# Kernel optimization log

Measured on AMD Instinct MI355X. Metric: run time of the kernel, lower is better.

## Reference

```python
import jax, jax.numpy as jnp
import numpy as np
from jax import lax

B, C_IN, C_MID, C_OUT, H, W = 8, 256, 128, 256, 128, 128
DN = ('NCHW', 'OIHW', 'NCHW')


def conv_bn(x, w, scale, shift, pad, relu):
    # conv (bias=False) + eval-mode BatchNorm folded to per-channel scale/shift
    y = lax.conv_general_dilated(x, w, (1, 1), [(pad, pad), (pad, pad)],
                                 dimension_numbers=DN)
    y = y * scale[None, :, None, None] + shift[None, :, None, None]
    return jax.nn.relu(y) if relu else y


def setup_inputs() -> dict:
    key = jax.random.key(0)
    ks = jax.random.split(key, 20)
    d = {"x": jax.random.normal(ks[0], (B, C_IN, H, W), dtype=jnp.float32)}
    f = 0.05  # weight scale
    def wparams(i, cout, cin, k):
        kk = jax.random.split(ks[i], 3)
        return (jax.random.normal(kk[0], (cout, cin, k, k), jnp.float32) * f,
                1.0 + 0.1 * jax.random.normal(kk[1], (cout,), jnp.float32),
                0.1 * jax.random.normal(kk[2], (cout,), jnp.float32))
    d["w_l"], d["s_l"], d["o_l"] = wparams(1, C_MID, C_IN, 3)
    d["w_r"], d["s_r"], d["o_r"] = wparams(2, C_MID, C_IN, 3)
    d["w_t"], d["s_t"], d["o_t"] = wparams(3, C_MID, C_IN, 3)
    d["w_b"], d["s_b"], d["o_b"] = wparams(4, C_MID, C_IN, 3)
    d["w2"], d["s2"], d["o2"] = wparams(5, C_OUT, C_MID, 3)
    d["w1"], d["s1"], d["o1"] = wparams(6, C_IN, C_IN, 1)
    return d


def reference(x, w_l, s_l, o_l, w_r, s_r, o_r, w_t, s_t, o_t,
              w_b, s_b, o_b, w2, s2, o2, w1, s1, o1):
    # four directional branches: conv+bn+relu then corner pooling (cummax scan)
    xl = lax.cummax(conv_bn(x, w_l, s_l, o_l, 1, True), axis=3, reverse=True)  # left: max over w'>=w
    xr = lax.cummax(conv_bn(x, w_r, s_r, o_r, 1, True), axis=3)                # right: max over w'<=w
    xt = lax.cummax(conv_bn(x, w_t, s_t, o_t, 1, True), axis=2, reverse=True)  # top: max over h'>=h
    xb = lax.cummax(conv_bn(x, w_b, s_b, o_b, 1, True), axis=2)                # bottom: max over h'<=h
    x1 = conv_bn(xl + xr + xb + xt, w2, s2, o2, 1, False)  # 3x3 conv+bn, no relu
    x2 = conv_bn(x, w1, s1, o1, 0, False)                  # 1x1 conv+bn skip, no relu
    return jax.nn.relu(x1 + x2)
```

## Files before the change

### kernel.cpp

```cpp
#include <hip/hip_runtime.h>

#define NEG_INF (-3.402823466e+38f)

typedef __bf16 bf16x8 __attribute__((ext_vector_type(8)));
typedef float  f32x16 __attribute__((ext_vector_type(16)));

__device__ __forceinline__ unsigned short f2bf(float f){
    unsigned u = __builtin_bit_cast(unsigned, f);
    u += 0x7fffu + ((u >> 16) & 1u);
    return (unsigned short)(u >> 16);
}
__device__ __forceinline__ float bf2f(unsigned short h){
    unsigned u = ((unsigned)h) << 16;
    return __builtin_bit_cast(float, u);
}

#if defined(__has_builtin)
#if __has_builtin(__builtin_amdgcn_global_load_lds)
#define ASYNC_CP 1
#endif
#endif

__device__ __forceinline__ void gl_lds(const unsigned short* g, unsigned short* lbase, int lane) {
#ifdef ASYNC_CP
    __builtin_amdgcn_global_load_lds(
        (const __attribute__((address_space(1))) unsigned int*)g,
        (__attribute__((address_space(3))) unsigned int*)lbase, 16, 0, 0);
#else
    *(uint4*)(lbase + (size_t)lane * 8) = *(const uint4*)g;
#endif
}

__global__ void __launch_bounds__(256)
k_xpose(const float* __restrict__ x, unsigned short* __restrict__ xh)
{
    __shared__ float tile[64 * 129];
    const int t = threadIdx.x;
    const int ci0 = blockIdx.x * 64, h = blockIdx.y, b = blockIdx.z;
    const float4* src = (const float4*)x;
#pragma unroll
    for (int i = 0; i < 8; ++i) {
        int idx = t + i * 256;
        int ci = idx >> 5, w4 = idx & 31;
        float4 v = src[((b * 256 + ci0 + ci) * 128 + h) * 32 + w4];
        tile[ci * 129 + w4 * 4 + 0] = v.x;
        tile[ci * 129 + w4 * 4 + 1] = v.y;
        tile[ci * 129 + w4 * 4 + 2] = v.z;
        tile[ci * 129 + w4 * 4 + 3] = v.w;
    }
    __syncthreads();
    unsigned* dst = (unsigned*)xh;
#pragma unroll
    for (int i = 0; i < 16; ++i) {
        int idx = t + i * 256;
        int w = idx >> 5, cp = idx & 31;
        float lo = tile[(cp * 2 + 0) * 129 + w];
        float hi = tile[(cp * 2 + 1) * 129 + w];
        dst[((b * 128 + h) * 128 + w) * 128 + (ci0 >> 1) + cp] =
            (unsigned)f2bf(lo) | ((unsigned)f2bf(hi) << 16);
    }
}

__global__ void __launch_bounds__(256)
k_wpack(const float* __restrict__ wl, const float* __restrict__ sl, const float* __restrict__ ol,
        const float* __restrict__ wr, const float* __restrict__ sr, const float* __restrict__ orr,
        const float* __restrict__ wt, const float* __restrict__ st, const float* __restrict__ ot,
        const float* __restrict__ wb, const float* __restrict__ sb, const float* __restrict__ ob,
        const float* __restrict__ w2, const float* __restrict__ s2, const float* __restrict__ o2,
        const float* __restrict__ w1, const float* __restrict__ s1, const float* __restrict__ o1,
        unsigned short* __restrict__ wpkBR, unsigned short* __restrict__ wpk2,
        unsigned short* __restrict__ wpk1, float* __restrict__ shF, float* __restrict__ obF)
{
    int i = blockIdx.x * 256 + threadIdx.x;
    if (i < 1179648) {
        int br = i / 294912, r = i % 294912;
        int c = r / 2304, r2 = r % 2304, ci = r2 / 9, k9 = r2 % 9;
        const float* wp = br == 0 ? wl : br == 1 ? wr : br == 2 ? wt : wb;
        const float* sp = br == 0 ? sl : br == 1 ? sr : br == 2 ? st : sb;
        float v = wp[r] * sp[c];
        int p = (c >> 4) * 64 + br * 16 + (c & 15);
        wpkBR[(((((ci >> 4) * 9 + k9) * 2 + ((ci >> 3) & 1)) * 512 + p) * 8) + (ci & 7)] = f2bf(v);
    } else if (i < 1474560) {
        int j = i - 1179648;
        int c = j / 1152, r2 = j % 1152, ci = r2 / 9, k9 = r2 % 9;
        wpk2[(((((ci >> 4) * 9 + k9) * 2 + ((ci >> 3) & 1)) * 256 + c) * 8) + (ci & 7)] = f2bf(w2[j] * s2[c]);
    } else if (i < 1540096) {
        int j = i - 1474560;
        int c = j >> 8, ci = j & 255;
        wpk1[((((ci >> 4) * 2 + ((ci >> 3) & 1)) * 256 + c) * 8) + (ci & 7)] = f2bf(w1[j] * s1[c]);
    } else if (i < 1540608) {
        int p = i - 1540096;
        int br = (p >> 4) & 3, c = (p >> 6) * 16 + (p & 15);
        const float* op = br == 0 ? ol : br == 1 ? orr : br == 2 ? ot : ob;
        shF[p] = op[c];
    } else if (i < 1540864) {
        int c = i - 1540608;
        obF[c] = o2[c] + o1[c];
    }
}

#define XIN_SH 12672
__global__ void __launch_bounds__(256, 2)
k_brconv(const unsigned short* __restrict__ xh, const unsigned short* __restrict__ wpkBR,
         const float* __restrict__ shF, unsigned short* __restrict__ sbuf2,
         unsigned short* __restrict__ ytbT, unsigned short* __restrict__ ytbB)
{
    __shared__ __align__(16) unsigned short smem[2 * XIN_SH + 128];
    unsigned short* xinA = smem;
    unsigned short* xinB = smem + XIN_SH;
    float* shs = (float*)(smem + 2 * XIN_SH);

    const int t = threadIdx.x;
    const int lin = (int)blockIdx.x + ((int)blockIdx.y << 3) + ((int)blockIdx.z << 8);
    const int swz = (lin & 7) * 256 + (lin >> 3);
    const int bx = swz & 7, h0 = ((swz >> 3) & 31) << 2, b = swz >> 8;
    const int wv = t >> 6, lane = t & 63;
    const int lo5 = lane & 31, hi1 = lane >> 5;
    const int hi32 = lane & 32;

    if (t < 64) shs[t] = shF[bx * 64 + t];
    for (int idx = t; idx < 3168; idx += 256)
        *(uint4*)(smem + idx * 8) = make_uint4(0, 0, 0, 0);

    f32x16 acc[2][4];
#pragma unroll
    for (int ct = 0; ct < 2; ++ct)
#pragma unroll
        for (int nb = 0; nb < 4; ++nb)
#pragma unroll
            for (int i = 0; i < 16; ++i) acc[ct][nb][i] = 0.f;

    __syncthreads();

    for (int s = wv; s < 24; s += 4) {
        int r = s >> 2, khi = (s >> 1) & 1, half = s & 1;
        int ih = h0 - 1 + r;
        if (ih >= 0 && ih < 128)
            gl_lds(xh + (((size_t)(b * 128 + ih) * 128 + half * 64 + lane) * 256) + khi * 8,
                   xinA + ((r * 2 + khi) * 132 + 1 + half * 64) * 8, lane);
    }
    __syncthreads();

    unsigned short* xcur = xinA;
    unsigned short* xnxt = xinB;

    for (int cb = 0; cb < 16; ++cb) {
        bf16x8 af0[9], af1[9];
        {
            const unsigned short* wp = wpkBR + ((size_t)(cb * 18 + hi1) * 512 + bx * 64) * 8;
#pragma unroll
            for (int k9 = 0; k9 < 9; ++k9) {
                af0[k9] = *(const bf16x8*)(wp + lo5 * 8);
                af1[k9] = *(const bf16x8*)(wp + (32 + lo5) * 8);
                wp += 8192;
            }
        }
        if (cb < 15) {
            const int nc = cb + 1;
            for (int s = wv; s < 24; s += 4) {
                int r = s >> 2, khi = (s >> 1) & 1, half = s & 1;
                int ih = h0 - 1 + r;
                if (ih >= 0 && ih < 128)
                    gl_lds(xh + (((size_t)(b * 128 + ih) * 128 + half * 64 + lane) * 256) + nc * 16 + khi * 8,
                           xnxt + ((r * 2 + khi) * 132 + 1 + half * 64) * 8, lane);
            }
        }
#pragma unroll
        for (int k9 = 0; k9 < 9; ++k9) {
            const int kh = k9 / 3, kw = k9 % 3;
#pragma unroll
            for (int nb = 0; nb < 4; ++nb) {
                bf16x8 bf = *(const bf16x8*)(xcur + (((wv + kh) * 2 + hi1) * 132 + nb * 32 + lo5 + kw) * 8);
                acc[0][nb] = __builtin_amdgcn_mfma_f32_32x32x16_bf16(af0[k9], bf, acc[0][nb], 0, 0, 0);
                acc[1][nb] = __builtin_amdgcn_mfma_f32_32x32x16_bf16(af1[k9], bf, acc[1][nb], 0, 0, 0);
            }
        }
        __syncthreads();
        unsigned short* tp = xcur; xcur = xnxt; xnxt = tp;
    }

    unsigned short* pbw = smem + wv * 3072;
    const int hg = h0 + wv;

#pragma unroll
    for (int r = 0; r < 8; ++r) {
        const int m = (r & 3) + 8 * (r >> 2) + 4 * hi1;
        const float shv = shs[m];
        float carry = NEG_INF;
#pragma unroll
        for (int nn = 3; nn >= 0; --nn) {
            float a = fmaxf(acc[0][nn][r] + shv, 0.f);
#pragma unroll
            for (int d = 1; d < 32; d <<= 1) {
                float o = __shfl_down(a, d);
                if (lo5 < 32 - d) a = fmaxf(a, o);
            }
            a = fmaxf(a, carry);
            carry = __shfl(a, hi32);
            acc[0][nn][r] = a;
        }
    }
#pragma unroll
    for (int r = 8; r < 16; ++r) {
        const int m = 16 + (r & 3) + 8 * ((r >> 2) & 1) + 4 * hi1;
        const float shv = shs[m];
        float carry = NEG_INF;
#pragma unroll
        for (int nn = 0; nn < 4; ++nn) {
            float a = fmaxf(acc[0][nn][r] + shv, 0.f);
#pragma unroll
            for (int d = 1; d < 32; d <<= 1) {
                float o = __shfl_up(a, d);
                if (lo5 >= d) a = fmaxf(a, o);
            }
            a = fmaxf(a, carry);
            carry = __shfl(a, hi32 | 31);
            acc[0][nn][r] = a;
        }
    }
#pragma unroll
    for (int r = 0; r < 8; ++r) {
        const int c16 = (r & 3) + 8 * (r >> 2) + 4 * hi1;
#pragma unroll
        for (int nn = 0; nn < 4; ++nn)
            pbw[(nn * 32 + lo5) * 24 + c16] = f2bf(acc[0][nn][r] + acc[0][nn][r + 8]);
    }
    {
        unsigned short* gdst = sbuf2 + ((size_t)(b * 128 + hg) * 128) * 128 + bx * 16;
#pragma unroll
        for (int i = 0; i < 4; ++i) {
            int idx = lane + i * 64;
            int w = idx >> 1, part = idx & 1;
            *(uint4*)(gdst + (size_t)w * 128 + part * 8) = *(const uint4*)(pbw + w * 24 + part * 8);
        }
    }
#pragma unroll
    for (int r = 0; r < 8; ++r) {
        const int c16 = (r & 3) + 8 * (r >> 2) + 4 * hi1;
        const float shv = shs[32 + c16];
#pragma unroll
        for (int nn = 0; nn < 4; ++nn)
            pbw[(nn * 32 + lo5) * 24 + c16] = f2bf(fmaxf(acc[1][nn][r] + shv, 0.f));
    }
    {
        unsigned short* gdst = ytbT + ((size_t)(b * 128 + hg) * 128) * 128 + bx * 16;
#pragma unroll
        for (int i = 0; i < 4; ++i) {
            int idx = lane + i * 64;
            int w = idx >> 1, part = idx & 1;
            *(uint4*)(gdst + (size_t)w * 128 + part * 8) = *(const uint4*)(pbw + w * 24 + part * 8);
        }
    }
#pragma unroll
    for (int r = 8; r < 16; ++r) {
        const int c16 = (r & 3) + 8 * ((r >> 2) & 1) + 4 * hi1;
        const float shv = shs[48 + c16];
#pragma unroll
        for (int nn = 0; nn < 4; ++nn)
            pbw[(nn * 32 + lo5) * 24 + c16] = f2bf(fmaxf(acc[1][nn][r] + shv, 0.f));
    }
    {
        unsigned short* gdst = ytbB + ((size_t)(b * 128 + hg) * 128) * 128 + bx * 16;
#pragma unroll
        for (int i = 0; i < 4; ++i) {
            int idx = lane + i * 64;
            int w = idx >> 1, part = idx & 1;
            *(uint4*)(gdst + (size_t)w * 128 + part * 8) = *(const uint4*)(pbw + w * 24 + part * 8);
        }
    }
}

template<int REV>
__global__ void __launch_bounds__(256)
k_colscan(const unsigned short* __restrict__ ytb, unsigned short* __restrict__ sbuf2)
{
    __shared__ float tile[8][8][33];
    const int t = threadIdx.x;
    const int w0 = blockIdx.x * 8, c0 = blockIdx.y * 32, b = blockIdx.z;
    const int sc = t & 31, sw = t >> 5;
    const int rh = t >> 5, r5 = t & 31;
    const int rw = r5 >> 2, rcq = r5 & 3;
    float cum = NEG_INF;
    for (int step = 0; step < 16; ++step) {
        int h0 = REV ? 120 - step * 8 : step * 8;
        for (int q = 0; q < 8; ++q) {
            int hh = REV ? 7 - q : q;
            int hg = h0 + hh;
            float v = bf2f(ytb[((b * 128 + hg) * 128 + (w0 + sw)) * 128 + c0 + sc]);
            cum = fmaxf(cum, v);
            tile[hh][sw][sc] = cum;
        }
        __syncthreads();
        {
            int hg = h0 + rh;
            unsigned short* p = sbuf2 + ((b * 128 + hg) * 128 + w0 + rw) * 128 + c0 + rcq * 8;
            uint4 u = *(uint4*)p;
            unsigned short* us = (unsigned short*)&u;
#pragma unroll
            for (int j = 0; j < 8; ++j)
                us[j] = f2bf(bf2f(us[j]) + tile[rh][rw][rcq * 8 + j]);
            *(uint4*)p = u;
        }
        __syncthreads();
    }
}

__global__ void __launch_bounds__(256, 2)
k_final(const unsigned short* __restrict__ sbuf2, const unsigned short* __restrict__ xh,
        const unsigned short* __restrict__ wpk2, const unsigned short* __restrict__ wpk1,
        const float* __restrict__ obF, float* __restrict__ out)
{
    __shared__ __align__(16) unsigned short smem[2 * XIN_SH + 128];
    unsigned short* xinA = smem;
    unsigned short* xinB = smem + XIN_SH;
    float* obs = (float*)(smem + 2 * XIN_SH);

    const int t = threadIdx.x;
    const int lin = (int)blockIdx.x + ((int)blockIdx.y << 2) + ((int)blockIdx.z << 7);
    const int swz = (lin & 7) * 128 + (lin >> 3);
    const int bx = swz & 3, h0 = ((swz >> 2) & 31) << 2, b = swz >> 7;
    const int wv = t >> 6, lane = t & 63;
    const int lo5 = lane & 31, hi1 = lane >> 5;

    if (t < 64) obs[t] = obF[bx * 64 + t];
    for (int idx = t; idx < 3168; idx += 256)
        *(uint4*)(smem + idx * 8) = make_uint4(0, 0, 0, 0);

    f32x16 acc[2][4];
#pragma unroll
    for (int ct = 0; ct < 2; ++ct)
#pragma unroll
        for (int nb = 0; nb < 4; ++nb)
#pragma unroll
            for (int i = 0; i < 16; ++i) acc[ct][nb][i] = 0.f;

    __syncthreads();

    for (int s = wv; s < 24; s += 4) {
        int r = s >> 2, khi = (s >> 1) & 1, half = s & 1;
        int ih = h0 - 1 + r;
        if (ih >= 0 && ih < 128)
            gl_lds(sbuf2 + (((size_t)(b * 128 + ih) * 128 + half * 64 + lane) * 128) + khi * 8,
                   xinA + ((r * 2 + khi) * 132 + 1 + half * 64) * 8, lane);
    }
    __syncthreads();

    unsigned short* xcur = xinA;
    unsigned short* xnxt = xinB;

    for (int cb = 0; cb < 8; ++cb) {
        bf16x8 af0[9], af1[9];
        {
            const unsigned short* wp = wpk2 + ((size_t)(cb * 18 + hi1) * 256 + bx * 64) * 8;
#pragma unroll
            for (int k9 = 0; k9 < 9; ++k9) {
                af0[k9] = *(const bf16x8*)(wp + lo5 * 8);
                af1[k9] = *(const bf16x8*)(wp + (32 + lo5) * 8);
                wp += 4096;
            }
        }
        if (cb < 7) {
            const int nc = cb + 1;
            for (int s = wv; s < 24; s += 4) {
                int r = s >> 2, khi = (s >> 1) & 1, half = s & 1;
                int ih = h0 - 1 + r;
                if (ih >= 0 && ih < 128)
                    gl_lds(sbuf2 + (((size_t)(b * 128 + ih) * 128 + half * 64 + lane) * 128) + nc * 16 + khi * 8,
                           xnxt + ((r * 2 + khi) * 132 + 1 + half * 64) * 8, lane);
            }
        }
#pragma unroll
        for (int k9 = 0; k9 < 9; ++k9) {
            const int kh = k9 / 3, kw = k9 % 3;
#pragma unroll
            for (int nb = 0; nb < 4; ++nb) {
                bf16x8 bf = *(const bf16x8*)(xcur + (((wv + kh) * 2 + hi1) * 132 + nb * 32 + lo5 + kw) * 8);
                acc[0][nb] = __builtin_amdgcn_mfma_f32_32x32x16_bf16(af0[k9], bf, acc[0][nb], 0, 0, 0);
                acc[1][nb] = __builtin_amdgcn_mfma_f32_32x32x16_bf16(af1[k9], bf, acc[1][nb], 0, 0, 0);
            }
        }
        __syncthreads();
        unsigned short* tp = xcur; xcur = xnxt; xnxt = tp;
    }

    {
        const unsigned short* xrow = xh + ((size_t)(b * 128 + h0 + wv) * 128) * 256 + hi1 * 8;
        const unsigned short* w1p  = wpk1 + ((size_t)hi1 * 256 + bx * 64) * 8;
#pragma unroll 4
        for (int cb = 0; cb < 16; ++cb) {
            bf16x8 a0 = *(const bf16x8*)(w1p + ((size_t)cb * 512 + lo5) * 8);
            bf16x8 a1 = *(const bf16x8*)(w1p + ((size_t)cb * 512 + 32 + lo5) * 8);
#pragma unroll
            for (int nb = 0; nb < 4; ++nb) {
                bf16x8 bf = *(const bf16x8*)(xrow + (size_t)(nb * 32 + lo5) * 256 + cb * 16);
                acc[0][nb] = __builtin_amdgcn_mfma_f32_32x32x16_bf16(a0, bf, acc[0][nb], 0, 0, 0);
                acc[1][nb] = __builtin_amdgcn_mfma_f32_32x32x16_bf16(a1, bf, acc[1][nb], 0, 0, 0);
            }
        }
    }

    const int hg = h0 + wv;
#pragma unroll
    for (int ct = 0; ct < 2; ++ct)
#pragma unroll
        for (int r = 0; r < 16; ++r) {
            const int m = ct * 32 + (r & 3) + 8 * (r >> 2) + 4 * hi1;
            const float bias = obs[m];
#pragma unroll
            for (int nb = 0; nb < 4; ++nb)
                out[((size_t)(b * 256 + bx * 64 + m) * 128 + hg) * 128 + nb * 32 + lo5] =
                    fmaxf(acc[ct][nb][r] + bias, 0.f);
        }
}

extern "C" void kernel_launch(void* const* d_in, const int* in_sizes, int n_in,
                              void* d_out, int out_size, void* d_ws, size_t ws_size,
                              hipStream_t stream)
{
    const float* x   = (const float*)d_in[0];
    const float* w_l = (const float*)d_in[1];
    const float* s_l = (const float*)d_in[2];
    const float* o_l = (const float*)d_in[3];
    const float* w_r = (const float*)d_in[4];
    const float* s_r = (const float*)d_in[5];
    const float* o_r = (const float*)d_in[6];
    const float* w_t = (const float*)d_in[7];
    const float* s_t = (const float*)d_in[8];
    const float* o_t = (const float*)d_in[9];
    const float* w_b = (const float*)d_in[10];
    const float* s_b = (const float*)d_in[11];
    const float* o_b = (const float*)d_in[12];
    const float* w2  = (const float*)d_in[13];
    const float* s2  = (const float*)d_in[14];
    const float* o2  = (const float*)d_in[15];
    const float* w1  = (const float*)d_in[16];
    const float* s1  = (const float*)d_in[17];
    const float* o1  = (const float*)d_in[18];
    float* out = (float*)d_out;
    char*  ws  = (char*)d_ws;

    unsigned short* xh    = (unsigned short*)(ws + 0);
    unsigned short* sbuf2 = (unsigned short*)(ws + 67108864);
    unsigned short* wpkBR = (unsigned short*)(ws + 100663296);
    unsigned short* wpk2  = (unsigned short*)(ws + 103022592);
    unsigned short* wpk1  = (unsigned short*)(ws + 103612416);
    float* shF = (float*)(ws + 103743488);
    float* obF = (float*)(ws + 103745536);

    unsigned short* ytbT = (unsigned short*)d_out;
    unsigned short* ytbB = ytbT + 16777216;

    dim3 blk(256);
    k_xpose<<<dim3(4, 128, 8), blk, 0, stream>>>(x, xh);
    k_wpack<<<dim3(6019), blk, 0, stream>>>(w_l, s_l, o_l, w_r, s_r, o_r,
                                            w_t, s_t, o_t, w_b, s_b, o_b,
                                            w2, s2, o2, w1, s1, o1,
                                            wpkBR, wpk2, wpk1, shF, obF);
    k_brconv<<<dim3(8, 32, 8), blk, 0, stream>>>(xh, wpkBR, shF, sbuf2, ytbT, ytbB);
    k_colscan<1><<<dim3(16, 4, 8), blk, 0, stream>>>(ytbT, sbuf2);
    k_colscan<0><<<dim3(16, 4, 8), blk, 0, stream>>>(ytbB, sbuf2);
    k_final<<<dim3(4, 32, 8), blk, 0, stream>>>(sbuf2, xh, wpk2, wpk1, obF, out);
}
```

Baseline: 710.6 us.

## Stage conv weights through LDS asynchronously and merge column-scan kernels

Both conv kernels now prefetch the per-channel-block weight fragments into a shared-memory buffer with async global-to-LDS copies, overlapped with the previous block's MFMA work, in place of direct global loads into registers each iteration. MFMA sections are wrapped in raised wave priority. The two column cummax-scan kernels are merged into one kernel that runs both directions per thread with simple strided scalar loads and no LDS tile. Risks include an extra barrier per iteration, more LDS per block that may hurt occupancy, and less coalesced 2-byte accesses in the scan.

After: 670.3 us. 5.7% less time.

```diff
diff --git a/kernel.cpp b/kernel.cpp
--- a/kernel.cpp
+++ b/kernel.cpp
@@ -100,15 +100,17 @@
 }
 
 #define XIN_SH 12672
+#define WBUF_SH 9216
 __global__ void __launch_bounds__(256, 2)
 k_brconv(const unsigned short* __restrict__ xh, const unsigned short* __restrict__ wpkBR,
          const float* __restrict__ shF, unsigned short* __restrict__ sbuf2,
          unsigned short* __restrict__ ytbT, unsigned short* __restrict__ ytbB)
 {
-    __shared__ __align__(16) unsigned short smem[2 * XIN_SH + 128];
+    __shared__ __align__(16) unsigned short smem[2 * XIN_SH + WBUF_SH + 128];
     unsigned short* xinA = smem;
     unsigned short* xinB = smem + XIN_SH;
-    float* shs = (float*)(smem + 2 * XIN_SH);
+    unsigned short* wbuf = smem + 2 * XIN_SH;
+    float* shs = (float*)(smem + 2 * XIN_SH + WBUF_SH);
 
     const int t = threadIdx.x;
     const int lin = (int)blockIdx.x + ((int)blockIdx.y << 3) + ((int)blockIdx.z << 8);
@@ -139,6 +141,8 @@
             gl_lds(xh + (((size_t)(b * 128 + ih) * 128 + half * 64 + lane) * 256) + khi * 8,
                    xinA + ((r * 2 + khi) * 132 + 1 + half * 64) * 8, lane);
     }
+    for (int s = wv; s < 18; s += 4)
+        gl_lds(wpkBR + ((size_t)s * 512 + bx * 64 + lane) * 8, wbuf + s * 512, lane);
     __syncthreads();
 
     unsigned short* xcur = xinA;
@@ -146,15 +150,13 @@
 
     for (int cb = 0; cb < 16; ++cb) {
         bf16x8 af0[9], af1[9];
-        {
-            const unsigned short* wp = wpkBR + ((size_t)(cb * 18 + hi1) * 512 + bx * 64) * 8;
-#pragma unroll
-            for (int k9 = 0; k9 < 9; ++k9) {
-                af0[k9] = *(const bf16x8*)(wp + lo5 * 8);
-                af1[k9] = *(const bf16x8*)(wp + (32 + lo5) * 8);
-                wp += 8192;
-            }
-        }
+#pragma unroll
+        for (int k9 = 0; k9 < 9; ++k9) {
+            af0[k9] = *(const bf16x8*)(wbuf + ((k9 * 2 + hi1) * 64 + lo5) * 8);
+            af1[k9] = *(const bf16x8*)(wbuf + ((k9 * 2 + hi1) * 64 + 32 + lo5) * 8);
+        }
+        __syncthreads();
+
         if (cb < 15) {
             const int nc = cb + 1;
             for (int s = wv; s < 24; s += 4) {
@@ -164,7 +166,12 @@
                     gl_lds(xh + (((size_t)(b * 128 + ih) * 128 + half * 64 + lane) * 256) + nc * 16 + khi * 8,
                            xnxt + ((r * 2 + khi) * 132 + 1 + half * 64) * 8, lane);
             }
-        }
+            for (int s = wv; s < 18; s += 4)
+                gl_lds(wpkBR + ((size_t)(nc * 18 + s) * 512 + bx * 64 + lane) * 8,
+                       wbuf + s * 512, lane);
+        }
+
+        __builtin_amdgcn_s_setprio(1);
 #pragma unroll
         for (int k9 = 0; k9 < 9; ++k9) {
             const int kh = k9 / 3, kw = k9 % 3;
@@ -175,6 +182,7 @@
                 acc[1][nb] = __builtin_amdgcn_mfma_f32_32x32x16_bf16(af1[k9], bf, acc[1][nb], 0, 0, 0);
             }
         }
+        __builtin_amdgcn_s_setprio(0);
         __syncthreads();
         unsigned short* tp = xcur; xcur = xnxt; xnxt = tp;
     }
@@ -270,38 +278,33 @@
     }
 }
 
-template<int REV>
 __global__ void __launch_bounds__(256)
-k_colscan(const unsigned short* __restrict__ ytb, unsigned short* __restrict__ sbuf2)
-{
-    __shared__ float tile[8][8][33];
+k_colscan2(const unsigned short* __restrict__ ytbT, const unsigned short* __restrict__ ytbB,
+           unsigned short* __restrict__ sbuf2)
+{
     const int t = threadIdx.x;
-    const int w0 = blockIdx.x * 8, c0 = blockIdx.y * 32, b = blockIdx.z;
-    const int sc = t & 31, sw = t >> 5;
-    const int rh = t >> 5, r5 = t & 31;
-    const int rw = r5 >> 2, rcq = r5 & 3;
-    float cum = NEG_INF;
-    for (int step = 0; step < 16; ++step) {
-        int h0 = REV ? 120 - step * 8 : step * 8;
-        for (int q = 0; q < 8; ++q) {
-            int hh = REV ? 7 - q : q;
-            int hg = h0 + hh;
-            float v = bf2f(ytb[((b * 128 + hg) * 128 + (w0 + sw)) * 128 + c0 + sc]);
-            cum = fmaxf(cum, v);
-            tile[hh][sw][sc] = cum;
-        }
-        __syncthreads();
-        {
-            int hg = h0 + rh;
-            unsigned short* p = sbuf2 + ((b * 128 + hg) * 128 + w0 + rw) * 128 + c0 + rcq * 8;
-            uint4 u = *(uint4*)p;
-            unsigned short* us = (unsigned short*)&u;
-#pragma unroll
-            for (int j = 0; j < 8; ++j)
-                us[j] = f2bf(bf2f(us[j]) + tile[rh][rw][rcq * 8 + j]);
-            *(uint4*)p = u;
-        }
-        __syncthreads();
+    const int b = blockIdx.x, wx = blockIdx.y;
+    const int w = wx * 2 + (t >> 7), c = t & 127;
+    const size_t hs = 128 * 128;
+    const size_t base = ((size_t)(b * 128) * 128 + w) * 128 + c;
+
+    {
+        float cum = NEG_INF;
+#pragma unroll 8
+        for (int h = 127; h >= 0; --h) {
+            cum = fmaxf(cum, bf2f(ytbT[base + (size_t)h * hs]));
+            unsigned short* p = sbuf2 + base + (size_t)h * hs;
+            *p = f2bf(bf2f(*p) + cum);
+        }
+    }
+    {
+        float cum = NEG_INF;
+#pragma unroll 8
+        for (int h = 0; h < 128; ++h) {
+            cum = fmaxf(cum, bf2f(ytbB[base + (size_t)h * hs]));
+            unsigned short* p = sbuf2 + base + (size_t)h * hs;
+            *p = f2bf(bf2f(*p) + cum);
+        }
     }
 }
 
@@ -310,10 +313,11 @@
         const unsigned short* __restrict__ wpk2, const unsigned short* __restrict__ wpk1,
         const float* __restrict__ obF, float* __restrict__ out)
 {
-    __shared__ __align__(16) unsigned short smem[2 * XIN_SH + 128];
+    __shared__ __align__(16) unsigned short smem[2 * XIN_SH + WBUF_SH + 128];
     unsigned short* xinA = smem;
     unsigned short* xinB = smem + XIN_SH;
-    float* obs = (float*)(smem + 2 * XIN_SH);
+    unsigned short* wbuf = smem + 2 * XIN_SH;
+    float* obs = (float*)(smem + 2 * XIN_SH + WBUF_SH);
 
     const int t = threadIdx.x;
     const int lin = (int)blockIdx.x + ((int)blockIdx.y << 2) + ((int)blockIdx.z << 7);
@@ -343,6 +347,8 @@
             gl_lds(sbuf2 + (((size_t)(b * 128 + ih) * 128 + half * 64 + lane) * 128) + khi * 8,
                    xinA + ((r * 2 + khi) * 132 + 1 + half * 64) * 8, lane);
     }
+    for (int s = wv; s < 18; s += 4)
+        gl_lds(wpk2 + ((size_t)s * 256 + bx * 64 + lane) * 8, wbuf + s * 512, lane);
     __syncthreads();
 
     unsigned short* xcur = xinA;
@@ -350,15 +356,13 @@
 
     for (int cb = 0; cb < 8; ++cb) {
         bf16x8 af0[9], af1[9];
-        {
-            const unsigned short* wp = wpk2 + ((size_t)(cb * 18 + hi1) * 256 + bx * 64) * 8;
-#pragma unroll
-            for (int k9 = 0; k9 < 9; ++k9) {
-                af0[k9] = *(const bf16x8*)(wp + lo5 * 8);
-                af1[k9] = *(const bf16x8*)(wp + (32 + lo5) * 8);
-                wp += 4096;
-            }
-        }
+#pragma unroll
+        for (int k9 = 0; k9 < 9; ++k9) {
+            af0[k9] = *(const bf16x8*)(wbuf + ((k9 * 2 + hi1) * 64 + lo5) * 8);
+            af1[k9] = *(const bf16x8*)(wbuf + ((k9 * 2 + hi1) * 64 + 32 + lo5) * 8);
+        }
+        __syncthreads();
+
         if (cb < 7) {
             const int nc = cb + 1;
             for (int s = wv; s < 24; s += 4) {
@@ -368,7 +372,12 @@
                     gl_lds(sbuf2 + (((size_t)(b * 128 + ih) * 128 + half * 64 + lane) * 128) + nc * 16 + khi * 8,
                            xnxt + ((r * 2 + khi) * 132 + 1 + half * 64) * 8, lane);
             }
-        }
+            for (int s = wv; s < 18; s += 4)
+                gl_lds(wpk2 + ((size_t)(nc * 18 + s) * 256 + bx * 64 + lane) * 8,
+                       wbuf + s * 512, lane);
+        }
+
+        __builtin_amdgcn_s_setprio(1);
 #pragma unroll
         for (int k9 = 0; k9 < 9; ++k9) {
             const int kh = k9 / 3, kw = k9 % 3;
@@ -379,6 +388,7 @@
                 acc[1][nb] = __builtin_amdgcn_mfma_f32_32x32x16_bf16(af1[k9], bf, acc[1][nb], 0, 0, 0);
             }
         }
+        __builtin_amdgcn_s_setprio(0);
         __syncthreads();
         unsigned short* tp = xcur; xcur = xnxt; xnxt = tp;
     }
@@ -457,7 +467,6 @@
                                             w2, s2, o2, w1, s1, o1,
                                             wpkBR, wpk2, wpk1, shF, obF);
     k_brconv<<<dim3(8, 32, 8), blk, 0, stream>>>(xh, wpkBR, shF, sbuf2, ytbT, ytbB);
-    k_colscan<1><<<dim3(16, 4, 8), blk, 0, stream>>>(ytbT, sbuf2);
-    k_colscan<0><<<dim3(16, 4, 8), blk, 0, stream>>>(ytbB, sbuf2);
+    k_colscan2<<<dim3(8, 64), blk, 0, stream>>>(ytbT, ytbB, sbuf2);
     k_final<<<dim3(4, 32, 8), blk, 0, stream>>>(sbuf2, xh, wpk2, wpk1, obF, out);
 }
```
